# Optimization experiments

Measured on AMD Instinct MI355X. Metric: run time of the kernel, lower is better.

The kernel has to match this reference:

```python
import jax, jax.numpy as jnp
import numpy as np
from jax import lax

DIM = 128
DIM_PREV = 64
DIM_NEXT = 256
HEADS = 4
HID = int(DIM * 2.66)  # 340
B, H, W = 8, 128, 128


def conv2d(x, w, stride=1, pad=0, groups=1):
    return lax.conv_general_dilated(
        x, w, (stride, stride), ((pad, pad), (pad, pad)),
        feature_group_count=groups,
        dimension_numbers=('NCHW', 'OIHW', 'NCHW'))


def layernorm_c(x, w, b):
    # WithBias LayerNorm over channel dim (unbiased=False var), eps=1e-5
    mu = x.mean(axis=1, keepdims=True)
    var = ((x - mu) ** 2).mean(axis=1, keepdims=True)
    return (x - mu) / jnp.sqrt(var + 1e-5) * w[None, :, None, None] + b[None, :, None, None]


def pixel_shuffle(x, r=2):
    b, c, h, w = x.shape
    co = c // (r * r)
    return x.reshape(b, co, r, r, h, w).transpose(0, 1, 4, 2, 5, 3).reshape(b, co, h * r, w * r)


def attention(x, temperature, qkv_w, qkv_dw_w, proj_w, heads):
    b, c, h, w = x.shape
    qkv = conv2d(conv2d(x, qkv_w), qkv_dw_w, pad=1, groups=3 * c)
    q, k, v = jnp.split(qkv, 3, axis=1)
    rs = lambda t: t.reshape(b, heads, c // heads, h * w)
    q, k, v = rs(q), rs(k), rs(v)
    q = q / jnp.maximum(jnp.linalg.norm(q, axis=-1, keepdims=True), 1e-12)
    k = k / jnp.maximum(jnp.linalg.norm(k, axis=-1, keepdims=True), 1e-12)
    # channel-wise attention: [b, heads, c/h, c/h]
    attn = jax.nn.softmax(jnp.einsum('bhcn,bhdn->bhcd', q, k) * temperature[None], axis=-1)
    out = jnp.einsum('bhcd,bhdn->bhcn', attn, v).reshape(b, c, h, w)
    return conv2d(out, proj_w)


def ffn(x, pin_w, dw_w, pout_w):
    x = conv2d(x, pin_w)
    x = conv2d(x, dw_w, pad=1, groups=x.shape[1])
    x1, x2 = jnp.split(x, 2, axis=1)
    return conv2d(jax.nn.gelu(x1, approximate=False) * x2, pout_w)


def setup_inputs() -> dict:
    key = jax.random.key(0)
    ks = jax.random.split(key, 16)
    s = 0.05
    return {
        'x_main': jax.random.normal(ks[0], (B, DIM, H, W), jnp.float32),
        'x_prev': jax.random.normal(ks[1], (B, DIM_PREV, 2 * H, 2 * W), jnp.float32),
        'x_next': jax.random.normal(ks[2], (B, DIM_NEXT, H // 2, W // 2), jnp.float32),
        'alpha_down': jnp.float32(0.5),
        'alpha_up': jnp.float32(0.5),
        'down_w': jax.random.normal(ks[3], (DIM, DIM_PREV, 3, 3), jnp.float32) * s,
        'up_w': jax.random.normal(ks[4], (DIM * 4, DIM_NEXT, 1, 1), jnp.float32) * s,
        'norm1_w': jnp.ones((DIM,), jnp.float32),
        'norm1_b': jnp.zeros((DIM,), jnp.float32),
        'temperature': jnp.ones((HEADS, 1, 1), jnp.float32),
        'qkv_w': jax.random.normal(ks[5], (3 * DIM, DIM, 1, 1), jnp.float32) * s,
        'qkv_dw_w': jax.random.normal(ks[6], (3 * DIM, 1, 3, 3), jnp.float32) * s,
        'proj_w': jax.random.normal(ks[7], (DIM, DIM, 1, 1), jnp.float32) * s,
        'norm2_w': jnp.ones((DIM,), jnp.float32),
        'norm2_b': jnp.zeros((DIM,), jnp.float32),
        'ffn_in_w': jax.random.normal(ks[8], (2 * HID, DIM, 1, 1), jnp.float32) * s,
        'ffn_dw_w': jax.random.normal(ks[9], (2 * HID, 1, 3, 3), jnp.float32) * s,
        'ffn_out_w': jax.random.normal(ks[10], (DIM, HID, 1, 1), jnp.float32) * s,
    }


def reference(x_main, x_prev, x_next, alpha_down, alpha_up, down_w, up_w,
              norm1_w, norm1_b, temperature, qkv_w, qkv_dw_w, proj_w,
              norm2_w, norm2_b, ffn_in_w, ffn_dw_w, ffn_out_w):
    f = x_main + alpha_down * conv2d(x_prev, down_w, stride=2, pad=1)
    f = f + alpha_up * pixel_shuffle(conv2d(x_next, up_w))
    x = attention(layernorm_c(f, norm1_w, norm1_b), temperature, qkv_w, qkv_dw_w, proj_w, HEADS)
    x = x_main + x
    x = x + ffn(layernorm_c(x, norm2_w, norm2_b), ffn_in_w, ffn_dw_w, ffn_out_w)
    return x
```

## Files before the change

### kernel.cpp

```cpp
#include <hip/hip_runtime.h>
#include <hip/hip_bf16.h>
#include <math.h>

using bf16 = __hip_bfloat16;
#define DEV static __device__ __forceinline__

typedef float    fx4   __attribute__((ext_vector_type(4)));
typedef float    fx2   __attribute__((ext_vector_type(2)));
typedef short    s16x8 __attribute__((ext_vector_type(8)));
typedef short    s16x4 __attribute__((ext_vector_type(4)));
typedef __bf16   bfx8  __attribute__((ext_vector_type(8)));
typedef unsigned int u32x4 __attribute__((ext_vector_type(4)));

constexpr int BATCH = 8;
constexpr int NPIX  = 16384;
constexpr int KFF   = 352;
constexpr int MFI   = 768;
constexpr int H1S   = 704;

DEV float uu2f(unsigned short u) { return __uint_as_float(((unsigned)u) << 16); }
DEV unsigned short f2us(float f) { bf16 h = __float2bfloat16(f); return *(unsigned short*)&h; }
DEV float bl2f(bf16 v) { return __bfloat162float(v); }

constexpr size_t OFF_SL1   = 0;
constexpr size_t OFF_XNEXT = OFF_SL1;
constexpr size_t OFF_UP    = OFF_SL1 + 16777216;
constexpr size_t OFF_XPREV = OFF_SL1 + 50331648;
constexpr size_t SZ_SL1    = 184549376;
constexpr size_t OFF_SL2   = OFF_SL1 + SZ_SL1;
constexpr size_t OFF_SL3   = OFF_SL2 + 100663296;
constexpr size_t OFF_SL4   = OFF_SL3 + 33554432;
constexpr size_t OFF_SL5   = OFF_SL4 + 33554432;
constexpr size_t OFF_W     = OFF_SL5 + 33554432;
constexpr size_t OFF_WUP   = OFF_W;
constexpr size_t OFF_WQKV  = OFF_W +  262144;
constexpr size_t OFF_WPRJ  = OFF_W +  360448;
constexpr size_t OFF_WFIN  = OFF_W +  393216;
constexpr size_t OFF_WFOUT = OFF_W +  589824;
constexpr size_t OFF_WTAP  = OFF_W +  679936;
constexpr size_t OFF_ZP    = OFF_W +  827392;
constexpr size_t OFF_NBUF  = OFF_W +  974848;
constexpr size_t OFF_S     = OFF_W +  983040;
constexpr size_t OFF_W2    = OFF_W + 1114112;

__global__ void conv_pad(const float* __restrict__ src, bf16* __restrict__ dst,
                         int Rs, int Cs, int Rd, int Cd)
{
    int n = Rd * Cd;
    for (int i = blockIdx.x * 256 + threadIdx.x; i < n; i += gridDim.x * 256) {
        int r = i / Cd, c = i % Cd;
        dst[i] = (r < Rs && c < Cs) ? __float2bfloat16(src[r * Cs + c]) : bf16(0.f);
    }
}

__global__ void wtap_prep(const float* __restrict__ src, bf16* __restrict__ dst)
{
    int i = blockIdx.x * 256 + threadIdx.x;
    if (i >= 9 * 128 * 64) return;
    int tap = i >> 13, rm = i & 8191, co = rm >> 6, ci = rm & 63;
    dst[i] = __float2bfloat16(src[(co * 64 + ci) * 9 + tap]);
}

__global__ __launch_bounds__(256) void transpose_c2p(
    const float* __restrict__ in, bf16* __restrict__ out, int C, int HW)
{
    __shared__ float ts[32][33];
    int hw0 = blockIdx.x * 32, c0 = blockIdx.y * 32, b = blockIdx.z;
    int rl = threadIdx.x >> 5, cl = threadIdx.x & 31;
#pragma unroll
    for (int i = 0; i < 4; i++)
        ts[rl + i * 8][cl] = in[((size_t)b * C + c0 + rl + i * 8) * HW + hw0 + cl];
    __syncthreads();
#pragma unroll
    for (int i = 0; i < 4; i++)
        out[((size_t)b * HW + hw0 + rl + i * 8) * C + c0 + cl] =
            __float2bfloat16(ts[cl][rl + i * 8]);
}

template <int EPI>
__global__ __launch_bounds__(256) void gemm_mfma(
    const bf16* __restrict__ Act, const bf16* __restrict__ Wt,
    int K, int Npb, int Mtrue, int Mstride, int Astride, int Aoff, int WtBS,
    bf16* __restrict__ outB,
    const float* __restrict__ xmain, bf16* __restrict__ x_out,
    const float* __restrict__ nw, const float* __restrict__ nb,
    const bf16* __restrict__ xres, float* __restrict__ outF)
{
    __shared__ short As[128 * 32];
    __shared__ short Bs[128 * 32];
    const int t = threadIdx.x;
    const int w = t >> 6, lane = t & 63;
    const int wr = w >> 1, wc = w & 1;
    const int lr = lane & 15, lg = lane >> 4;
    const int n0 = blockIdx.x * 128;
    const int m0 = blockIdx.y * 128;
    const int b  = blockIdx.z;
    const bf16* Abase = Act + (size_t)b * Npb * Astride + Aoff;
    const bf16* Wtb   = Wt + (size_t)b * WtBS;

    fx4 acc[4][4];
#pragma unroll
    for (int i = 0; i < 4; i++)
#pragma unroll
        for (int j = 0; j < 4; j++) acc[i][j] = fx4{0.f, 0.f, 0.f, 0.f};

    const int f0 = w * 128 + lane, f1 = f0 + 64;
    const int r0 = f0 >> 2, c0 = (f0 & 3) * 8;
    const int r1 = f1 >> 2, c1 = (f1 & 3) * 8;

    for (int ks = 0; ks < K; ks += 32) {
        __builtin_amdgcn_global_load_lds(
            (const __attribute__((address_space(1))) void*)(Abase + (size_t)(n0 + r0) * Astride + ks + c0),
            (__attribute__((address_space(3))) void*)(As + w * 1024), 16, 0, 0);
        __builtin_amdgcn_global_load_lds(
            (const __attribute__((address_space(1))) void*)(Abase + (size_t)(n0 + r1) * Astride + ks + c1),
            (__attribute__((address_space(3))) void*)(As + w * 1024 + 512), 16, 0, 0);
        __builtin_amdgcn_global_load_lds(
            (const __attribute__((address_space(1))) void*)(Wtb + (size_t)(m0 + r0) * K + ks + c0),
            (__attribute__((address_space(3))) void*)(Bs + w * 1024), 16, 0, 0);
        __builtin_amdgcn_global_load_lds(
            (const __attribute__((address_space(1))) void*)(Wtb + (size_t)(m0 + r1) * K + ks + c1),
            (__attribute__((address_space(3))) void*)(Bs + w * 1024 + 512), 16, 0, 0);
        __syncthreads();
        bfx8 af[4], bw[4];
#pragma unroll
        for (int mi = 0; mi < 4; mi++)
            af[mi] = __builtin_bit_cast(bfx8,
                *(const s16x8*)&As[(wr * 64 + mi * 16 + lr) * 32 + lg * 8]);
#pragma unroll
        for (int ni = 0; ni < 4; ni++)
            bw[ni] = __builtin_bit_cast(bfx8,
                *(const s16x8*)&Bs[(wc * 64 + ni * 16 + lr) * 32 + lg * 8]);
#pragma unroll
        for (int mi = 0; mi < 4; mi++)
#pragma unroll
            for (int ni = 0; ni < 4; ni++)
                acc[mi][ni] = __builtin_amdgcn_mfma_f32_16x16x32_bf16(
                    af[mi], bw[ni], acc[mi][ni], 0, 0, 0);
        __syncthreads();
    }

    if (EPI == 0) {
#pragma unroll
        for (int mi = 0; mi < 4; mi++)
#pragma unroll
            for (int ni = 0; ni < 4; ni++) {
                int co = m0 + wc * 64 + ni * 16 + lr;
                if (co < Mtrue) {
#pragma unroll
                    for (int r = 0; r < 4; r++) {
                        int px = n0 + wr * 64 + mi * 16 + lg * 4 + r;
                        outB[((size_t)b * Npb + px) * Mstride + co] =
                            __float2bfloat16(acc[mi][ni][r]);
                    }
                }
            }
    } else if (EPI == 1) {
        float xv[4][4][4];
#pragma unroll
        for (int mi = 0; mi < 4; mi++)
#pragma unroll
            for (int ni = 0; ni < 4; ni++) {
                int co = wc * 64 + ni * 16 + lr;
                fx4 x4 = *(const fx4*)&xmain[((size_t)b * 128 + co) * 16384 +
                                             n0 + wr * 64 + mi * 16 + lg * 4];
#pragma unroll
                for (int r = 0; r < 4; r++) xv[mi][ni][r] = x4[r] + acc[mi][ni][r];
            }
        __shared__ float ps[2][128];
        __shared__ float pss[2][128];
#pragma unroll
        for (int mi = 0; mi < 4; mi++)
#pragma unroll
            for (int r = 0; r < 4; r++) {
                float s = 0.f, s2 = 0.f;
#pragma unroll
                for (int ni = 0; ni < 4; ni++) {
                    float v = xv[mi][ni][r]; s += v; s2 += v * v;
                }
#pragma unroll
                for (int m = 1; m < 16; m <<= 1) {
                    s  += __shfl_xor(s, m);
                    s2 += __shfl_xor(s2, m);
                }
                if (lr == 0) {
                    int row = wr * 64 + mi * 16 + lg * 4 + r;
                    ps[wc][row] = s; pss[wc][row] = s2;
                }
            }
        __syncthreads();
        float nwv[4], nbv[4];
#pragma unroll
        for (int ni = 0; ni < 4; ni++) {
            int co = wc * 64 + ni * 16 + lr;
            nwv[ni] = nw[co]; nbv[ni] = nb[co];
        }
#pragma unroll
        for (int mi = 0; mi < 4; mi++)
#pragma unroll
            for (int r = 0; r < 4; r++) {
                int row = wr * 64 + mi * 16 + lg * 4 + r;
                float s  = ps[0][row] + ps[1][row];
                float s2 = pss[0][row] + pss[1][row];
                float mu = s * (1.f / 128.f);
                float var = s2 * (1.f / 128.f) - mu * mu;
                float rstd = rsqrtf(var + 1e-5f);
                size_t px = (size_t)b * 16384 + n0 + row;
#pragma unroll
                for (int ni = 0; ni < 4; ni++) {
                    int co = wc * 64 + ni * 16 + lr;
                    float v = xv[mi][ni][r];
                    x_out[px * 128 + co] = __float2bfloat16(v);
                    outB[px * 128 + co] = __float2bfloat16((v - mu) * rstd * nwv[ni] + nbv[ni]);
                }
            }
    } else {
#pragma unroll
        for (int mi = 0; mi < 4; mi++)
#pragma unroll
            for (int ni = 0; ni < 4; ni++) {
                int co = wc * 64 + ni * 16 + lr;
                int pxb = n0 + wr * 64 + mi * 16 + lg * 4;
                fx4 o;
#pragma unroll
                for (int r = 0; r < 4; r++)
                    o[r] = acc[mi][ni][r] +
                           bl2f(xres[((size_t)b * 16384 + pxb + r) * 128 + co]);
                *(fx4*)&outF[((size_t)b * 128 + co) * 16384 + pxb] = o;
            }
    }
}

template <int REMAP>
__global__ __launch_bounds__(256) void gemm_mloop(
    const bf16* __restrict__ Act, const bf16* __restrict__ Wt,
    int nM, int Mtrue, int Mstride, bf16* __restrict__ outB)
{
    __shared__ short As[16384];
    __shared__ short Bs[16384];
    const int t = threadIdx.x;
    const int w = t >> 6, lane = t & 63;
    const int wr = w >> 1, wc = w & 1;
    const int lr = lane & 15, lg = lane >> 4;
    const int n0 = blockIdx.x * 128;
    const int b  = blockIdx.y;
    const short* Abase = (const short*)Act + (size_t)b * NPIX * 128;

#pragma unroll
    for (int i = 0; i < 8; i++) {
        int chunk = i * 256 + w * 64 + lane;
        int kb = chunk >> 9, row = (chunk >> 2) & 127, c8 = chunk & 3;
        __builtin_amdgcn_global_load_lds(
            (const __attribute__((address_space(1))) void*)
                (Abase + (size_t)(n0 + row) * 128 + kb * 32 + c8 * 8),
            (__attribute__((address_space(3))) void*)(As + i * 2048 + w * 512), 16, 0, 0);
    }

    for (int mt = 0; mt < nM; mt++) {
#pragma unroll
        for (int i = 0; i < 8; i++) {
            int chunk = i * 256 + w * 64 + lane;
            int kb = chunk >> 9, row = (chunk >> 2) & 127, c8 = chunk & 3;
            __builtin_amdgcn_global_load_lds(
                (const __attribute__((address_space(1))) void*)
                    ((const short*)Wt + (size_t)(mt * 128 + row) * 128 + kb * 32 + c8 * 8),
                (__attribute__((address_space(3))) void*)(Bs + i * 2048 + w * 512), 16, 0, 0);
        }
        __syncthreads();
        fx4 acc[4][4];
#pragma unroll
        for (int i = 0; i < 4; i++)
#pragma unroll
            for (int j = 0; j < 4; j++) acc[i][j] = fx4{0.f, 0.f, 0.f, 0.f};
#pragma unroll
        for (int ks = 0; ks < 4; ks++) {
            bfx8 af[4], bw[4];
#pragma unroll
            for (int mi = 0; mi < 4; mi++)
                af[mi] = __builtin_bit_cast(bfx8,
                    *(const s16x8*)&As[ks * 4096 + (wr * 64 + mi * 16 + lr) * 32 + lg * 8]);
#pragma unroll
            for (int ni = 0; ni < 4; ni++)
                bw[ni] = __builtin_bit_cast(bfx8,
                    *(const s16x8*)&Bs[ks * 4096 + (wc * 64 + ni * 16 + lr) * 32 + lg * 8]);
#pragma unroll
            for (int mi = 0; mi < 4; mi++)
#pragma unroll
                for (int ni = 0; ni < 4; ni++)
                    acc[mi][ni] = __builtin_amdgcn_mfma_f32_16x16x32_bf16(
                        af[mi], bw[ni], acc[mi][ni], 0, 0, 0);
        }
        __syncthreads();
#pragma unroll
        for (int mi = 0; mi < 4; mi++)
#pragma unroll
            for (int ni = 0; ni < 4; ni++) {
                int co = mt * 128 + wc * 64 + ni * 16 + lr;
                if (co < Mtrue) {
                    int cd = (REMAP && co >= 340) ? co + 12 : co;
#pragma unroll
                    for (int r = 0; r < 4; r++) {
                        int px = n0 + wr * 64 + mi * 16 + lg * 4 + r;
                        outB[((size_t)b * NPIX + px) * Mstride + cd] =
                            __float2bfloat16(acc[mi][ni][r]);
                    }
                    if (REMAP && co >= 340 && co < 352) {
#pragma unroll
                        for (int r = 0; r < 4; r++) {
                            int px = n0 + wr * 64 + mi * 16 + lg * 4 + r;
                            outB[((size_t)b * NPIX + px) * Mstride + co] = bf16(0.f);
                        }
                    }
                } else if (REMAP && co < 692) {
#pragma unroll
                    for (int r = 0; r < 4; r++) {
                        int px = n0 + wr * 64 + mi * 16 + lg * 4 + r;
                        outB[((size_t)b * NPIX + px) * Mstride + co + 12] = bf16(0.f);
                    }
                }
            }
    }
}

__global__ __launch_bounds__(256) void down_mfma_ln(
    const bf16* __restrict__ xprev_pm,
    const float* __restrict__ xmain,
    const bf16* __restrict__ up_pm,
    const bf16* __restrict__ wtap,
    const float* __restrict__ alpha_d, const float* __restrict__ alpha_u,
    const float* __restrict__ n1w, const float* __restrict__ n1b,
    const bf16* __restrict__ zeropage,
    bf16* __restrict__ y1)
{
    __shared__ short As[128 * 64];
    __shared__ short Bs[128 * 64];
    __shared__ float ps[2][128];
    __shared__ float pss[2][128];
    const int t = threadIdx.x;
    const int w = t >> 6, lane = t & 63;
    const int wr = w >> 1, wc = w & 1;
    const int lr = lane & 15, lg = lane >> 4;
    const int y = blockIdx.x;
    const int b = blockIdx.y;

    const int srow0 = 32 * w + (lane >> 3);
    const int sci8  = lane & 7;
    const short* wtbase = (const short*)wtap;

    fx4 acc[4][4];
#pragma unroll
    for (int i = 0; i < 4; i++)
#pragma unroll
        for (int j = 0; j < 4; j++) acc[i][j] = fx4{0.f, 0.f, 0.f, 0.f};

#pragma unroll
    for (int tap = 0; tap < 9; tap++) {
        const int dy = tap / 3, dx = tap % 3;
        const int iy = 2 * y - 1 + dy;
        const bool rowok = (iy >= 0) && (iy < 256);
        const short* arow = (const short*)xprev_pm +
                            (((size_t)b * 65536 + (size_t)iy * 256) * 64);
#pragma unroll
        for (int i = 0; i < 4; i++) {
            int row = srow0 + 8 * i;
            int ix = 2 * row - 1 + dx;
            const short* src = (rowok && ix >= 0 && ix < 256)
                                 ? (arow + (size_t)ix * 64 + sci8 * 8)
                                 : (const short*)zeropage;
            __builtin_amdgcn_global_load_lds(
                (const __attribute__((address_space(1))) void*)src,
                (__attribute__((address_space(3))) void*)(As + w * 2048 + i * 512), 16, 0, 0);
            __builtin_amdgcn_global_load_lds(
                (const __attribute__((address_space(1))) void*)
                    (wtbase + tap * 8192 + w * 2048 + i * 512 + lane * 8),
                (__attribute__((address_space(3))) void*)(Bs + w * 2048 + i * 512), 16, 0, 0);
        }
        __syncthreads();
        bfx8 af[4][2], bw[4][2];
#pragma unroll
        for (int mi = 0; mi < 4; mi++)
#pragma unroll
            for (int ks = 0; ks < 2; ks++)
                af[mi][ks] = __builtin_bit_cast(bfx8,
                    *(const s16x8*)&As[(wr * 64 + mi * 16 + lr) * 64 + ks * 32 + lg * 8]);
#pragma unroll
        for (int ni = 0; ni < 4; ni++)
#pragma unroll
            for (int ks = 0; ks < 2; ks++)
                bw[ni][ks] = __builtin_bit_cast(bfx8,
                    *(const s16x8*)&Bs[(wc * 64 + ni * 16 + lr) * 64 + ks * 32 + lg * 8]);
#pragma unroll
        for (int mi = 0; mi < 4; mi++)
#pragma unroll
            for (int ni = 0; ni < 4; ni++)
#pragma unroll
                for (int ks = 0; ks < 2; ks++)
                    acc[mi][ni] = __builtin_amdgcn_mfma_f32_16x16x32_bf16(
                        af[mi][ks], bw[ni][ks], acc[mi][ni], 0, 0, 0);
        __syncthreads();
    }

    const float ad = alpha_d[0], au = alpha_u[0];
    const int n2base = (y >> 1) * 64;
    const int chb2 = (y & 1) * 2;
    float fv[4][4][4];
#pragma unroll
    for (int mi = 0; mi < 4; mi++) {
        const int x0 = wr * 64 + mi * 16 + lg * 4;
#pragma unroll
        for (int ni = 0; ni < 4; ni++) {
            const int co = wc * 64 + ni * 16 + lr;
            fx4 xm = *(const fx4*)&xmain[(((size_t)b * 128 + co) * 128 + y) * 128 + x0];
            const short* uprow = (const short*)up_pm +
                ((size_t)b * 4096 + n2base + (x0 >> 1)) * 512 + co * 4 + chb2;
            unsigned up01 = *(const unsigned*)uprow;
            unsigned up23 = *(const unsigned*)(uprow + 512);
            fv[mi][ni][0] = xm[0] + ad * acc[mi][ni][0] + au * uu2f((unsigned short)(up01 & 0xffff));
            fv[mi][ni][1] = xm[1] + ad * acc[mi][ni][1] + au * uu2f((unsigned short)(up01 >> 16));
            fv[mi][ni][2] = xm[2] + ad * acc[mi][ni][2] + au * uu2f((unsigned short)(up23 & 0xffff));
            fv[mi][ni][3] = xm[3] + ad * acc[mi][ni][3] + au * uu2f((unsigned short)(up23 >> 16));
        }
    }
#pragma unroll
    for (int mi = 0; mi < 4; mi++)
#pragma unroll
        for (int r = 0; r < 4; r++) {
            float s = 0.f, s2 = 0.f;
#pragma unroll
            for (int ni = 0; ni < 4; ni++) {
                float v = fv[mi][ni][r]; s += v; s2 += v * v;
            }
#pragma unroll
            for (int m = 1; m < 16; m <<= 1) {
                s  += __shfl_xor(s, m);
                s2 += __shfl_xor(s2, m);
            }
            if (lr == 0) {
                int row = wr * 64 + mi * 16 + lg * 4 + r;
                ps[wc][row] = s; pss[wc][row] = s2;
            }
        }
    __syncthreads();
    float nwv[4], nbv[4];
#pragma unroll
    for (int ni = 0; ni < 4; ni++) {
        int co = wc * 64 + ni * 16 + lr;
        nwv[ni] = n1w[co]; nbv[ni] = n1b[co];
    }
#pragma unroll
    for (int mi = 0; mi < 4; mi++)
#pragma unroll
        for (int r = 0; r < 4; r++) {
            int row = wr * 64 + mi * 16 + lg * 4 + r;
            float s  = ps[0][row] + ps[1][row];
            float s2 = pss[0][row] + pss[1][row];
            float mu = s * (1.f / 128.f);
            float var = s2 * (1.f / 128.f) - mu * mu;
            float rstd = rsqrtf(var + 1e-5f);
            size_t px = (size_t)b * 16384 + (size_t)y * 128 + row;
#pragma unroll
            for (int ni = 0; ni < 4; ni++) {
                int co = wc * 64 + ni * 16 + lr;
                ((short*)y1)[px * 128 + co] =
                    (short)f2us((fv[mi][ni][r] - mu) * rstd * nwv[ni] + nbv[ni]);
            }
        }
}

template <int YT2>
DEV void dw_accum(const short* __restrict__ L, const float* __restrict__ swb,
                  int x, int yh, int lofs, fx2 acc[YT2][4])
{
    fx2 wreg[9][4];
#pragma unroll
    for (int tap = 0; tap < 9; tap++)
#pragma unroll
        for (int k = 0; k < 4; k++)
            wreg[tap][k] = *(const fx2*)&swb[tap * 32 + lofs + 2 * k];
#pragma unroll
    for (int yy = 0; yy < YT2; yy++)
#pragma unroll
        for (int k = 0; k < 4; k++) acc[yy][k] = fx2{0.f, 0.f};
#pragma unroll
    for (int r = 0; r < YT2 + 2; r++) {
        fx2 rv[3][4];
#pragma unroll
        for (int dxp = 0; dxp < 3; dxp++) {
            s16x8 raw = *(const s16x8*)&L[((yh * YT2 + r) * 34 + x + dxp) * 40 + lofs];
            u32x4 u = __builtin_bit_cast(u32x4, raw);
#pragma unroll
            for (int k = 0; k < 4; k++)
                rv[dxp][k] = fx2{__uint_as_float(u[k] << 16),
                                 __uint_as_float(u[k] & 0xffff0000u)};
        }
#pragma unroll
        for (int yy = 0; yy < YT2; yy++) {
            int dy = r - yy;
            if (dy < 0 || dy > 2) continue;
#pragma unroll
            for (int dx = 0; dx < 3; dx++)
#pragma unroll
                for (int k = 0; k < 4; k++)
                    acc[yy][k] += rv[dx][k] * wreg[dy * 3 + dx][k];
        }
    }
}

template <int GATE, int QKNORM, int YTILE>
__global__ __launch_bounds__(256) void dw_conv(
    const bf16* __restrict__ in, const float* __restrict__ w,
    bf16* __restrict__ out, float* __restrict__ nbuf)
{
    constexpr int CHST  = GATE ? 704 : 384;
    constexpr int CHOST = GATE ? 352 : 384;
    constexpr int NROWS = YTILE + 2;
    constexpr int YT2   = YTILE / 2;
    constexpr int LSZ   = NROWS * 34 * 40;
    __shared__ short L1[LSZ];
    __shared__ short L2[GATE ? LSZ : 8];
    __shared__ float sw1[288];
    __shared__ float sw2[GATE ? 288 : 8];
    __shared__ float snorm[QKNORM ? 32 : 8];
    const int t = threadIdx.x;
    const int x = t & 31, chg = (t >> 5) & 3, yh = t >> 7;
    const int cg = blockIdx.y, b = blockIdx.z;
    const int x0 = (blockIdx.x & 3) * 32, y0 = (blockIdx.x >> 2) * YTILE;

    if (QKNORM && t < 32) snorm[t] = 0.f;
    if (GATE) {
        for (int i = t; i < 288; i += 256) {
            int c = i & 31, tap = i >> 5;
            int cr = cg * 32 + c;
            sw1[i] = (cr < 340) ? w[cr * 9 + tap] : 0.f;
            sw2[i] = (cr < 340) ? w[(cr + 340) * 9 + tap] : 0.f;
        }
    } else {
        for (int i = t; i < 288; i += 256) {
            int c = i & 31, tap = i >> 5;
            sw1[i] = w[(cg * 32 + c) * 9 + tap];
        }
    }
    const short* bin = (const short*)in + (size_t)b * NPIX * CHST + cg * 32;
    constexpr int NCHK1 = NROWS * 136;
    const int NCHK = GATE ? 2 * NCHK1 : NCHK1;
    for (int id = t; id < NCHK; id += 256) {
        int half = 0, idd = id;
        if (GATE && idd >= NCHK1) { half = 1; idd -= NCHK1; }
        int row = idd / 136, rm = idd % 136, pos = rm >> 2, c8 = rm & 3;
        int gy = y0 - 1 + row, gx = x0 - 1 + pos;
        s16x8 v = s16x8{0, 0, 0, 0, 0, 0, 0, 0};
        if (gy >= 0 && gy < 128 && gx >= 0 && gx < 128)
            v = *(const s16x8*)(bin + ((size_t)(gy << 7) + gx) * CHST + half * 352 + c8 * 8);
        short* dst = (GATE && half) ? L2 : L1;
        *(s16x8*)&dst[(row * 34 + pos) * 40 + c8 * 8] = v;
    }
    __syncthreads();

    const int lofs = chg * 8;
    fx2 a1[YT2][4];
    dw_accum<YT2>(L1, sw1, x, yh, lofs, a1);
    if (GATE) {
#pragma unroll
        for (int yy = 0; yy < YT2; yy++)
#pragma unroll
            for (int k = 0; k < 4; k++) {
                fx2 v = a1[yy][k];
#pragma unroll
                for (int e = 0; e < 2; e++) {
                    float xx = v[e];
                    float x2 = xx * xx;
                    float mzz = xx * fmaf(-0.1029432f, x2, -2.3022082f);
                    float un = exp2f(mzz);
                    v[e] = xx * __builtin_amdgcn_rcpf(1.f + un);
                }
                a1[yy][k] = v;
            }
        fx2 a2[YT2][4];
        dw_accum<YT2>(L2, sw2, x, yh, lofs, a2);
#pragma unroll
        for (int yy = 0; yy < YT2; yy++)
#pragma unroll
            for (int k = 0; k < 4; k++) a1[yy][k] *= a2[yy][k];
    }

    if (QKNORM && cg < 8) {
        fx2 sq[4];
#pragma unroll
        for (int k = 0; k < 4; k++) {
            sq[k] = fx2{0.f, 0.f};
#pragma unroll
            for (int yy = 0; yy < YT2; yy++) sq[k] += a1[yy][k] * a1[yy][k];
        }
#pragma unroll
        for (int m = 1; m < 32; m <<= 1)
#pragma unroll
            for (int k = 0; k < 4; k++) {
                sq[k][0] += __shfl_xor(sq[k][0], m);
                sq[k][1] += __shfl_xor(sq[k][1], m);
            }
        if (x == 0) {
#pragma unroll
            for (int k = 0; k < 4; k++) {
                atomicAdd(&snorm[chg * 8 + 2 * k],     sq[k][0]);
                atomicAdd(&snorm[chg * 8 + 2 * k + 1], sq[k][1]);
            }
        }
    }

#pragma unroll
    for (int yy = 0; yy < YT2; yy++) {
        s16x8 pk;
#pragma unroll
        for (int k = 0; k < 4; k++) {
            pk[2 * k]     = (short)f2us(a1[yy][k][0]);
            pk[2 * k + 1] = (short)f2us(a1[yy][k][1]);
        }
        *(s16x8*)((short*)out + (((size_t)b * NPIX) + ((y0 + yh * YT2 + yy) << 7) + x0 + x) * CHOST
                  + cg * 32 + chg * 8) = pk;
    }

    if (QKNORM) {
        __syncthreads();
        if (cg < 8 && t < 32)
            atomicAdd(&nbuf[b * 256 + cg * 32 + t], snorm[t]);
    }
}

__global__ __launch_bounds__(256) void scores(const bf16* __restrict__ qkv,
                                              float* __restrict__ S)
{
    __shared__ short qs[256 * 40];
    __shared__ short ks2[256 * 40];
    const int t = threadIdx.x;
    const int bh = blockIdx.x, b = bh >> 2, h = bh & 3;
    const int n0 = blockIdx.y * 256;
    {
        const short* src = (const short*)qkv + ((size_t)(b * 16384 + n0 + t)) * 384 + h * 32;
#pragma unroll
        for (int i = 0; i < 4; i++) {
            *(s16x8*)&qs[t * 40 + i * 8]  = *(const s16x8*)(src + i * 8);
            *(s16x8*)&ks2[t * 40 + i * 8] = *(const s16x8*)(src + 128 + i * 8);
        }
    }
    __syncthreads();
    const int i2 = t >> 4, j16 = t & 15;
    float a00 = 0.f, a01 = 0.f, a10 = 0.f, a11 = 0.f;
    for (int n = 0; n < 256; n++) {
        unsigned qq = *(const unsigned*)&qs[n * 40 + i2 * 2];
        unsigned kk = *(const unsigned*)&ks2[n * 40 + j16 * 2];
        float q0 = uu2f((unsigned short)(qq & 0xffff)), q1 = uu2f((unsigned short)(qq >> 16));
        float k0 = uu2f((unsigned short)(kk & 0xffff)), k1 = uu2f((unsigned short)(kk >> 16));
        a00 = fmaf(q0, k0, a00); a01 = fmaf(q0, k1, a01);
        a10 = fmaf(q1, k0, a10); a11 = fmaf(q1, k1, a11);
    }
    float* base = S + (size_t)bh * 1024;
    atomicAdd(&base[(i2 * 2 + 0) * 32 + j16 * 2 + 0], a00);
    atomicAdd(&base[(i2 * 2 + 0) * 32 + j16 * 2 + 1], a01);
    atomicAdd(&base[(i2 * 2 + 1) * 32 + j16 * 2 + 0], a10);
    atomicAdd(&base[(i2 * 2 + 1) * 32 + j16 * 2 + 1], a11);
}

__global__ void softmax_k(float* __restrict__ S, const float* __restrict__ nbuf,
                          const float* __restrict__ temp)
{
    __shared__ float invk[32];
    int bh = blockIdx.x, b = bh >> 2, h = bh & 3, i = threadIdx.x;
    invk[i] = 1.f / fmaxf(sqrtf(nbuf[b * 256 + 128 + h * 32 + i]), 1e-12f);
    __syncthreads();
    float ti = temp[h] / fmaxf(sqrtf(nbuf[b * 256 + h * 32 + i]), 1e-12f);
    float* row = S + (size_t)bh * 1024 + i * 32;
    float vals[32], m = -1e30f;
#pragma unroll
    for (int j = 0; j < 32; j++) { vals[j] = row[j] * ti * invk[j]; m = fmaxf(m, vals[j]); }
    float s = 0.f;
#pragma unroll
    for (int j = 0; j < 32; j++) { vals[j] = expf(vals[j] - m); s += vals[j]; }
    float r = 1.f / s;
#pragma unroll
    for (int j = 0; j < 32; j++) row[j] = vals[j] * r;
}

__global__ __launch_bounds__(256) void attn_fold(
    const bf16* __restrict__ Wprj, const float* __restrict__ S, bf16* __restrict__ W2)
{
    __shared__ float sS[4096];
    const int b = blockIdx.x, t = threadIdx.x;
    for (int i = t; i < 4096; i += 256) sS[i] = S[b * 4096 + i];
    __syncthreads();
    const int co = t >> 1, jh = t & 1;
    const short* prow = (const short*)Wprj + co * 128 + jh * 64;
    float p[64];
#pragma unroll
    for (int i = 0; i < 8; i++) {
        s16x8 v = *(const s16x8*)(prow + i * 8);
#pragma unroll
        for (int e = 0; e < 8; e++) p[i * 8 + e] = uu2f((unsigned short)v[e]);
    }
    short outv[64];
#pragma unroll
    for (int h2 = 0; h2 < 2; h2++) {
        const int h = jh * 2 + h2;
        const float* Sh = &sS[h * 1024];
#pragma unroll 4
        for (int d = 0; d < 32; d++) {
            float a = 0.f;
#pragma unroll
            for (int c = 0; c < 32; c++) a = fmaf(p[h2 * 32 + c], Sh[c * 32 + d], a);
            outv[h2 * 32 + d] = (short)f2us(a);
        }
    }
    short* dst = (short*)W2 + (size_t)b * 16384 + co * 128 + jh * 64;
#pragma unroll
    for (int i = 0; i < 8; i++) *(s16x8*)(dst + i * 8) = *(s16x8*)&outv[i * 8];
}

extern "C" void kernel_launch(void* const* d_in, const int* in_sizes, int n_in,
                              void* d_out, int out_size, void* d_ws, size_t ws_size,
                              hipStream_t stream)
{
    const float* x_main      = (const float*)d_in[0];
    const float* x_prev      = (const float*)d_in[1];
    const float* x_next      = (const float*)d_in[2];
    const float* alpha_down  = (const float*)d_in[3];
    const float* alpha_up    = (const float*)d_in[4];
    const float* down_w      = (const float*)d_in[5];
    const float* up_w        = (const float*)d_in[6];
    const float* norm1_w     = (const float*)d_in[7];
    const float* norm1_b     = (const float*)d_in[8];
    const float* temperature = (const float*)d_in[9];
    const float* qkv_w       = (const float*)d_in[10];
    const float* qkv_dw_w    = (const float*)d_in[11];
    const float* proj_w      = (const float*)d_in[12];
    const float* norm2_w     = (const float*)d_in[13];
    const float* norm2_b     = (const float*)d_in[14];
    const float* ffn_in_w    = (const float*)d_in[15];
    const float* ffn_dw_w    = (const float*)d_in[16];
    const float* ffn_out_w   = (const float*)d_in[17];
    float* out = (float*)d_out;
    (void)in_sizes; (void)n_in; (void)out_size; (void)ws_size;

    char* ws = (char*)d_ws;
    bf16* xnext_pm = (bf16*)(ws + OFF_XNEXT);
    bf16* up_pm    = (bf16*)(ws + OFF_UP);
    bf16* xprev_pm = (bf16*)(ws + OFF_XPREV);
    bf16* qkv_a    = (bf16*)(ws + OFF_SL1);
    bf16* h1       = (bf16*)(ws + OFF_SL1);
    bf16* qkv_b    = (bf16*)(ws + OFF_SL2);
    bf16* gbuf     = (bf16*)(ws + OFF_SL2);
    bf16* y1       = (bf16*)(ws + OFF_SL3);
    bf16* x_pm     = (bf16*)(ws + OFF_SL4);
    bf16* y2       = (bf16*)(ws + OFF_SL5);
    bf16* Wup      = (bf16*)(ws + OFF_WUP);
    bf16* Wqkv     = (bf16*)(ws + OFF_WQKV);
    bf16* Wprj     = (bf16*)(ws + OFF_WPRJ);
    bf16* Wfin     = (bf16*)(ws + OFF_WFIN);
    bf16* Wfout    = (bf16*)(ws + OFF_WFOUT);
    bf16* Wtap     = (bf16*)(ws + OFF_WTAP);
    bf16* zpage    = (bf16*)(ws + OFF_ZP);
    float* nbuf    = (float*)(ws + OFF_NBUF);
    float* Sbuf    = (float*)(ws + OFF_S);
    bf16* W2buf    = (bf16*)(ws + OFF_W2);

    hipMemsetAsync(nbuf, 0, 8192 + 131072, stream);
    hipMemsetAsync(zpage, 0, 256, stream);

    conv_pad<<<dim3(512), 256, 0, stream>>>(up_w, Wup, 512, 256, 512, 256);
    conv_pad<<<dim3(192), 256, 0, stream>>>(qkv_w, Wqkv, 384, 128, 384, 128);
    conv_pad<<<dim3(64), 256, 0, stream>>>(proj_w, Wprj, 128, 128, 128, 128);
    conv_pad<<<dim3(384), 256, 0, stream>>>(ffn_in_w, Wfin, 680, 128, MFI, 128);
    conv_pad<<<dim3(176), 256, 0, stream>>>(ffn_out_w, Wfout, 128, 340, 128, KFF);
    wtap_prep<<<dim3(288), 256, 0, stream>>>(down_w, Wtap);

    transpose_c2p<<<dim3(128, 8, BATCH), 256, 0, stream>>>(x_next, xnext_pm, 256, 4096);
    transpose_c2p<<<dim3(2048, 2, BATCH), 256, 0, stream>>>(x_prev, xprev_pm, 64, 65536);

    gemm_mfma<0><<<dim3(32, 4, BATCH), 256, 0, stream>>>(
        xnext_pm, Wup, 256, 4096, 512, 512, 256, 0, 0, up_pm,
        nullptr, nullptr, nullptr, nullptr, nullptr, nullptr);

    down_mfma_ln<<<dim3(128, BATCH), 256, 0, stream>>>(
        xprev_pm, x_main, up_pm, Wtap, alpha_down, alpha_up, norm1_w, norm1_b,
        zpage, y1);

    gemm_mloop<0><<<dim3(128, BATCH), 256, 0, stream>>>(y1, Wqkv, 3, 384, 384, qkv_a);

    dw_conv<0, 1, 8><<<dim3(64, 12, BATCH), 256, 0, stream>>>(qkv_a, qkv_dw_w, qkv_b, nbuf);

    scores<<<dim3(32, 64), 256, 0, stream>>>(qkv_b, Sbuf);
    softmax_k<<<dim3(32), 32, 0, stream>>>(Sbuf, nbuf, temperature);
    attn_fold<<<dim3(BATCH), 256, 0, stream>>>(Wprj, Sbuf, W2buf);

    gemm_mfma<1><<<dim3(128, 1, BATCH), 256, 0, stream>>>(
        qkv_b, W2buf, 128, NPIX, 128, 128, 384, 256, 16384, y2,
        x_main, x_pm, norm2_w, norm2_b, nullptr, nullptr);

    gemm_mloop<1><<<dim3(128, BATCH), 256, 0, stream>>>(y2, Wfin, 6, 680, H1S, h1);

    dw_conv<1, 0, 4><<<dim3(128, 11, BATCH), 256, 0, stream>>>(h1, ffn_dw_w, gbuf, nullptr);

    gemm_mfma<2><<<dim3(128, 1, BATCH), 256, 0, stream>>>(
        gbuf, Wfout, KFF, NPIX, 128, 128, KFF, 0, 0, nullptr,
        nullptr, nullptr, nullptr, nullptr, x_pm, out);
}
```

Before: 594.3 us.

## Merge prep kernels, fuse softmax into fold, vectorize x_prev transpose, repad dw LDS

```diff
diff --git a/kernel.cpp b/kernel.cpp
--- a/kernel.cpp
+++ b/kernel.cpp
@@ -43,23 +43,42 @@
 constexpr size_t OFF_S     = OFF_W +  983040;
 constexpr size_t OFF_W2    = OFF_W + 1114112;
 
-__global__ void conv_pad(const float* __restrict__ src, bf16* __restrict__ dst,
-                         int Rs, int Cs, int Rd, int Cd)
-{
-    int n = Rd * Cd;
-    for (int i = blockIdx.x * 256 + threadIdx.x; i < n; i += gridDim.x * 256) {
-        int r = i / Cd, c = i % Cd;
-        dst[i] = (r < Rs && c < Cs) ? __float2bfloat16(src[r * Cs + c]) : bf16(0.f);
-    }
-}
-
-__global__ void wtap_prep(const float* __restrict__ src, bf16* __restrict__ dst)
+__global__ void prep_all(const float* __restrict__ up_w, const float* __restrict__ qkv_w,
+                         const float* __restrict__ proj_w, const float* __restrict__ ffn_in_w,
+                         const float* __restrict__ ffn_out_w, const float* __restrict__ down_w,
+                         bf16* __restrict__ Wup, bf16* __restrict__ Wqkv, bf16* __restrict__ Wprj,
+                         bf16* __restrict__ Wfin, bf16* __restrict__ Wfout, bf16* __restrict__ Wtap,
+                         float* __restrict__ zf, bf16* __restrict__ zpage)
 {
     int i = blockIdx.x * 256 + threadIdx.x;
-    if (i >= 9 * 128 * 64) return;
-    int tap = i >> 13, rm = i & 8191, co = rm >> 6, ci = rm & 63;
-    dst[i] = __float2bfloat16(src[(co * 64 + ci) * 9 + tap]);
-}
+    if (i < 131072) { Wup[i] = __float2bfloat16(up_w[i]); return; }
+    i -= 131072;
+    if (i < 49152) { Wqkv[i] = __float2bfloat16(qkv_w[i]); return; }
+    i -= 49152;
+    if (i < 16384) { Wprj[i] = __float2bfloat16(proj_w[i]); return; }
+    i -= 16384;
+    if (i < 98304) {
+        Wfin[i] = (i < 680 * 128) ? __float2bfloat16(ffn_in_w[i]) : bf16(0.f);
+        return;
+    }
+    i -= 98304;
+    if (i < 45056) {
+        int r = i / KFF, c = i % KFF;
+        Wfout[i] = (c < 340) ? __float2bfloat16(ffn_out_w[r * 340 + c]) : bf16(0.f);
+        return;
+    }
+    i -= 45056;
+    if (i < 73728) {
+        int tap = i >> 13, rm = i & 8191, co = rm >> 6, ci = rm & 63;
+        Wtap[i] = __float2bfloat16(down_w[(co * 64 + ci) * 9 + tap]);
+        return;
+    }
+    i -= 73728;
+    if (i < 34816) { zf[i] = 0.f; return; }
+    i -= 34816;
+    if (i < 128) zpage[i] = bf16(0.f);
+}
+constexpr int PREP_TOT = 131072 + 49152 + 16384 + 98304 + 45056 + 73728 + 34816 + 128;
 
 __global__ __launch_bounds__(256) void transpose_c2p(
     const float* __restrict__ in, bf16* __restrict__ out, int C, int HW)
@@ -75,6 +94,25 @@
     for (int i = 0; i < 4; i++)
         out[((size_t)b * HW + hw0 + rl + i * 8) * C + c0 + cl] =
             __float2bfloat16(ts[cl][rl + i * 8]);
+}
+
+__global__ __launch_bounds__(256) void transpose_prev(
+    const float* __restrict__ in, bf16* __restrict__ out)
+{
+    __shared__ float ts[64][33];
+    const int hw0 = blockIdx.x * 32, b = blockIdx.y;
+    const int cl = threadIdx.x >> 5, hl = threadIdx.x & 31;
+#pragma unroll
+    for (int i = 0; i < 8; i++) {
+        int c = i * 8 + cl;
+        ts[c][hl] = in[((size_t)b * 64 + c) * 65536 + hw0 + hl];
+    }
+    __syncthreads();
+    const int hw = threadIdx.x >> 3, c8 = (threadIdx.x & 7) * 8;
+    s16x8 pk;
+#pragma unroll
+    for (int e = 0; e < 8; e++) pk[e] = (short)f2us(ts[c8 + e][hw]);
+    *(s16x8*)((short*)out + ((size_t)b * 65536 + hw0 + hw) * 64 + c8) = pk;
 }
 
 template <int EPI>
@@ -486,7 +524,7 @@
         fx2 rv[3][4];
 #pragma unroll
         for (int dxp = 0; dxp < 3; dxp++) {
-            s16x8 raw = *(const s16x8*)&L[((yh * YT2 + r) * 34 + x + dxp) * 40 + lofs];
+            s16x8 raw = *(const s16x8*)&L[((yh * YT2 + r) * 34 + x + dxp) * 44 + lofs];
             u32x4 u = __builtin_bit_cast(u32x4, raw);
 #pragma unroll
             for (int k = 0; k < 4; k++)
@@ -515,7 +553,7 @@
     constexpr int CHOST = GATE ? 352 : 384;
     constexpr int NROWS = YTILE + 2;
     constexpr int YT2   = YTILE / 2;
-    constexpr int LSZ   = NROWS * 34 * 40;
+    constexpr int LSZ   = NROWS * 34 * 44;
     __shared__ short L1[LSZ];
     __shared__ short L2[GATE ? LSZ : 8];
     __shared__ float sw1[288];
@@ -523,8 +561,9 @@
     __shared__ float snorm[QKNORM ? 32 : 8];
     const int t = threadIdx.x;
     const int x = t & 31, chg = (t >> 5) & 3, yh = t >> 7;
-    const int cg = blockIdx.y, b = blockIdx.z;
-    const int x0 = (blockIdx.x & 3) * 32, y0 = (blockIdx.x >> 2) * YTILE;
+    const int cg = blockIdx.x, b = blockIdx.z;
+    const int sp = blockIdx.y;
+    const int x0 = (sp & 3) * 32, y0 = (sp >> 2) * YTILE;
 
     if (QKNORM && t < 32) snorm[t] = 0.f;
     if (GATE) {
@@ -552,7 +591,7 @@
         if (gy >= 0 && gy < 128 && gx >= 0 && gx < 128)
             v = *(const s16x8*)(bin + ((size_t)(gy << 7) + gx) * CHST + half * 352 + c8 * 8);
         short* dst = (GATE && half) ? L2 : L1;
-        *(s16x8*)&dst[(row * 34 + pos) * 40 + c8 * 8] = v;
+        *(s16x8*)&dst[(row * 34 + pos) * 44 + c8 * 8] = v;
     }
     __syncthreads();
 
@@ -660,32 +699,34 @@
     atomicAdd(&base[(i2 * 2 + 1) * 32 + j16 * 2 + 1], a11);
 }
 
-__global__ void softmax_k(float* __restrict__ S, const float* __restrict__ nbuf,
-                          const float* __restrict__ temp)
-{
-    __shared__ float invk[32];
-    int bh = blockIdx.x, b = bh >> 2, h = bh & 3, i = threadIdx.x;
-    invk[i] = 1.f / fmaxf(sqrtf(nbuf[b * 256 + 128 + h * 32 + i]), 1e-12f);
+__global__ __launch_bounds__(256) void softmax_fold(
+    const float* __restrict__ S, const float* __restrict__ nbuf,
+    const float* __restrict__ temp, const bf16* __restrict__ Wprj,
+    bf16* __restrict__ W2)
+{
+    __shared__ float sS[4096];
+    __shared__ float sinv[256];
+    const int b = blockIdx.x, t = threadIdx.x;
+    sinv[t] = 1.f / fmaxf(sqrtf(nbuf[b * 256 + t]), 1e-12f);
+    for (int i = t; i < 4096; i += 256) sS[i] = S[b * 4096 + i];
     __syncthreads();
-    float ti = temp[h] / fmaxf(sqrtf(nbuf[b * 256 + h * 32 + i]), 1e-12f);
-    float* row = S + (size_t)bh * 1024 + i * 32;
-    float vals[32], m = -1e30f;
-#pragma unroll
-    for (int j = 0; j < 32; j++) { vals[j] = row[j] * ti * invk[j]; m = fmaxf(m, vals[j]); }
-    float s = 0.f;
-#pragma unroll
-    for (int j = 0; j < 32; j++) { vals[j] = expf(vals[j] - m); s += vals[j]; }
-    float r = 1.f / s;
-#pragma unroll
-    for (int j = 0; j < 32; j++) row[j] = vals[j] * r;
-}
-
-__global__ __launch_bounds__(256) void attn_fold(
-    const bf16* __restrict__ Wprj, const float* __restrict__ S, bf16* __restrict__ W2)
-{
-    __shared__ float sS[4096];
-    const int b = blockIdx.x, t = threadIdx.x;
-    for (int i = t; i < 4096; i += 256) sS[i] = S[b * 4096 + i];
+    if (t < 128) {
+        int h = t >> 5, i = t & 31;
+        float ti = temp[h] * sinv[h * 32 + i];
+        float* row = &sS[h * 1024 + i * 32];
+        float vals[32], m = -1e30f;
+#pragma unroll
+        for (int j = 0; j < 32; j++) {
+            float v = row[j] * ti * sinv[128 + h * 32 + j];
+            vals[j] = v; m = fmaxf(m, v);
+        }
+        float s = 0.f;
+#pragma unroll
+        for (int j = 0; j < 32; j++) { vals[j] = expf(vals[j] - m); s += vals[j]; }
+        float r = 1.f / s;
+#pragma unroll
+        for (int j = 0; j < 32; j++) row[j] = vals[j] * r;
+    }
     __syncthreads();
     const int co = t >> 1, jh = t & 1;
     const short* prow = (const short*)Wprj + co * 128 + jh * 64;
@@ -761,18 +802,12 @@
     float* Sbuf    = (float*)(ws + OFF_S);
     bf16* W2buf    = (bf16*)(ws + OFF_W2);
 
-    hipMemsetAsync(nbuf, 0, 8192 + 131072, stream);
-    hipMemsetAsync(zpage, 0, 256, stream);
-
-    conv_pad<<<dim3(512), 256, 0, stream>>>(up_w, Wup, 512, 256, 512, 256);
-    conv_pad<<<dim3(192), 256, 0, stream>>>(qkv_w, Wqkv, 384, 128, 384, 128);
-    conv_pad<<<dim3(64), 256, 0, stream>>>(proj_w, Wprj, 128, 128, 128, 128);
-    conv_pad<<<dim3(384), 256, 0, stream>>>(ffn_in_w, Wfin, 680, 128, MFI, 128);
-    conv_pad<<<dim3(176), 256, 0, stream>>>(ffn_out_w, Wfout, 128, 340, 128, KFF);
-    wtap_prep<<<dim3(288), 256, 0, stream>>>(down_w, Wtap);
+    prep_all<<<dim3((PREP_TOT + 255) / 256), 256, 0, stream>>>(
+        up_w, qkv_w, proj_w, ffn_in_w, ffn_out_w, down_w,
+        Wup, Wqkv, Wprj, Wfin, Wfout, Wtap, nbuf, zpage);
 
     transpose_c2p<<<dim3(128, 8, BATCH), 256, 0, stream>>>(x_next, xnext_pm, 256, 4096);
-    transpose_c2p<<<dim3(2048, 2, BATCH), 256, 0, stream>>>(x_prev, xprev_pm, 64, 65536);
+    transpose_prev<<<dim3(2048, BATCH), 256, 0, stream>>>(x_prev, xprev_pm);
 
     gemm_mfma<0><<<dim3(32, 4, BATCH), 256, 0, stream>>>(
         xnext_pm, Wup, 256, 4096, 512, 512, 256, 0, 0, up_pm,
@@ -784,11 +819,10 @@
 
     gemm_mloop<0><<<dim3(128, BATCH), 256, 0, stream>>>(y1, Wqkv, 3, 384, 384, qkv_a);
 
-    dw_conv<0, 1, 8><<<dim3(64, 12, BATCH), 256, 0, stream>>>(qkv_a, qkv_dw_w, qkv_b, nbuf);
+    dw_conv<0, 1, 8><<<dim3(12, 64, BATCH), 256, 0, stream>>>(qkv_a, qkv_dw_w, qkv_b, nbuf);
 
     scores<<<dim3(32, 64), 256, 0, stream>>>(qkv_b, Sbuf);
-    softmax_k<<<dim3(32), 32, 0, stream>>>(Sbuf, nbuf, temperature);
-    attn_fold<<<dim3(BATCH), 256, 0, stream>>>(Wprj, Sbuf, W2buf);
+    softmax_fold<<<dim3(BATCH), 256, 0, stream>>>(Sbuf, nbuf, temperature, Wprj, W2buf);
 
     gemm_mfma<1><<<dim3(128, 1, BATCH), 256, 0, stream>>>(
         qkv_b, W2buf, 128, NPIX, 128, 128, 384, 256, 16384, y2,
@@ -796,7 +830,7 @@
 
     gemm_mloop<1><<<dim3(128, BATCH), 256, 0, stream>>>(y2, Wfin, 6, 680, H1S, h1);
 
-    dw_conv<1, 0, 4><<<dim3(128, 11, BATCH), 256, 0, stream>>>(h1, ffn_dw_w, gbuf, nullptr);
+    dw_conv<1, 0, 4><<<dim3(11, 128, BATCH), 256, 0, stream>>>(h1, ffn_dw_w, gbuf, nullptr);
 
     gemm_mfma<2><<<dim3(128, 1, BATCH), 256, 0, stream>>>(
         gbuf, Wfout, KFF, NPIX, 128, 128, KFF, 0, 0, nullptr,
```

After: 678.6 us. 14.2% more time.
